# Performance work log

Hardware: AMD Instinct MI355X
Metric: run time of the kernel (lower is better)

## Reference

```python
import jax, jax.numpy as jnp
import numpy as np
import math

INPUT_DIM = 1024
DIM_K = 1024
DIM_V = 1024
B, N = 4, 2048

def setup_inputs() -> dict:
    key = jax.random.key(0)
    ks = jax.random.split(key, 7)
    s = 1.0 / math.sqrt(INPUT_DIM)
    return {
        'x':  jax.random.normal(ks[0], (B, N, INPUT_DIM), dtype=jnp.float32),
        'Wq': jax.random.uniform(ks[1], (DIM_K, INPUT_DIM), jnp.float32, -s, s),
        'bq': jax.random.uniform(ks[2], (DIM_K,), jnp.float32, -s, s),
        'Wk': jax.random.uniform(ks[3], (DIM_K, INPUT_DIM), jnp.float32, -s, s),
        'bk': jax.random.uniform(ks[4], (DIM_K,), jnp.float32, -s, s),
        'Wv': jax.random.uniform(ks[5], (DIM_V, INPUT_DIM), jnp.float32, -s, s),
        'bv': jax.random.uniform(ks[6], (DIM_V,), jnp.float32, -s, s),
    }

def reference(x, Wq, bq, Wk, bk, Wv, bv):
    norm_fact = 1.0 / math.sqrt(DIM_K)
    # torch Linear: y = x @ W.T + b
    Q = jnp.einsum('bnd,kd->bnk', x, Wq) + bq  # [B,N,dim_k]
    K = jnp.einsum('bnd,kd->bnk', x, Wk) + bk  # [B,N,dim_k]
    V = jnp.einsum('bnd,vd->bnv', x, Wv) + bv  # [B,N,dim_v]
    scores = jnp.einsum('bqk,bnk->bqn', Q, K)  # [B,N,N]
    # NOTE: original code applies softmax FIRST, then scales by norm_fact
    atten = jax.nn.softmax(scores, axis=-1) * norm_fact
    return jnp.einsum('bqn,bnv->bqv', atten, V)  # [B,N,dim_v]
```

## Files before the change

### kernel.cpp

```cpp
#include <hip/hip_runtime.h>


typedef _Float16 hfx8 __attribute__((ext_vector_type(8)));
typedef _Float16 hfx4 __attribute__((ext_vector_type(4)));
typedef float fx4 __attribute__((ext_vector_type(4)));

__device__ __forceinline__ void load_lds16(const void* g, void* l) {
    __builtin_amdgcn_global_load_lds(
        (const __attribute__((address_space(1))) void*)g,
        (__attribute__((address_space(3))) void*)l, 16, 0, 0);
}

template <int N> __device__ __forceinline__ void vmwait() {
    if constexpr (N == 8) asm volatile("s_waitcnt vmcnt(8)" ::: "memory");
    else asm volatile("s_waitcnt vmcnt(0)" ::: "memory");
}

__device__ __forceinline__ void xcd_remap(int& x, int& y, int& z) {
    const int gx = gridDim.x, gy = gridDim.y;
    const int lin = blockIdx.x + gx * (blockIdx.y + gy * blockIdx.z);
    const int cpx = (gx * gy * gridDim.z) >> 3;
    const int w = (lin & 7) * cpx + (lin >> 3);
    x = w % gx;
    y = (w / gx) % gy;
    z = w / (gx * gy);
}

__global__ __launch_bounds__(256) void conv_all_kernel(
    const float4* __restrict__ x, _Float16* __restrict__ xs,
    const float4* __restrict__ w0, const float4* __restrict__ w1, const float4* __restrict__ w2,
    _Float16* __restrict__ o0, _Float16* __restrict__ o1, _Float16* __restrict__ o2)
{
    const int b = blockIdx.x;
    const float4* in;
    _Float16* out;
    long i;
    if (b < 8192) {
        in = x; out = xs;
        i = (long)b * 256 + threadIdx.x;
    } else {
        const int wi = b - 8192;
        const int wsel = wi >> 10;
        in = wsel == 0 ? w0 : (wsel == 1 ? w1 : w2);
        out = wsel == 0 ? o0 : (wsel == 1 ? o1 : o2);
        i = (long)(wi & 1023) * 256 + threadIdx.x;
    }
    float4 v = in[i];
    hfx4 h;
    h[0] = (_Float16)v.x; h[1] = (_Float16)v.y;
    h[2] = (_Float16)v.z; h[3] = (_Float16)v.w;
    *(hfx4*)&out[i * 4] = h;
}

template <int OMODE>
__global__ __launch_bounds__(256, 2) void gemm2(
    const _Float16* __restrict__ A,
    const _Float16* __restrict__ Bq, const _Float16* __restrict__ Bk, const _Float16* __restrict__ Bv,
    const float* __restrict__ bq, const float* __restrict__ bk, const float* __restrict__ bv,
    float* __restrict__ outF, _Float16* __restrict__ oQ, _Float16* __restrict__ oK, _Float16* __restrict__ oV,
    int K, int lda, int ldb, int ldc, float alpha,
    long sAz, long sBz, long sCz)
{
    constexpr int BM = 128, BN = 128, BK = 64;
    constexpr int LPT = 8;

    __shared__ __attribute__((aligned(16))) _Float16 lds[2][(BM + BN) * BK];

    int bx, by, z;
    xcd_remap(bx, by, z);

    A += (long)z * sAz;
    const _Float16* B = (OMODE == 1) ? (z == 0 ? Bq : (z == 1 ? Bk : Bv))
                                     : Bq + (long)z * sBz;

    const int tid = threadIdx.x;
    const int lane = tid & 63;
    const int wv = tid >> 6;
    const int wr = wv >> 1, wc = wv & 1;
    const int lr = lane & 15, lk = lane >> 4;

    const long m0 = (long)by * BM;
    const long n0 = (long)bx * BN;

    fx4 acc[4][4] = {};

    auto STAGE = [&](int kt, int b) {
#pragma unroll
        for (int i = 0; i < LPT; ++i) {
            const int c = i * 256 + tid;
            if (i < 4) {
                const int row = c >> 3, slot = c & 7;
                load_lds16(A + (m0 + row) * (long)lda + kt + ((slot ^ (row & 7)) << 3),
                           &lds[b][c * 8]);
            } else {
                const int c2 = c - 1024;
                const int row = c2 >> 3, slot = c2 & 7;
                load_lds16(B + (n0 + row) * (long)ldb + kt + ((slot ^ (row & 7)) << 3),
                           &lds[b][BM * BK + c2 * 8]);
            }
        }
    };

    const int NT = K / BK;
    STAGE(0, 0);
    STAGE(BK, 1);
    vmwait<8>();
    __builtin_amdgcn_s_barrier();
    __builtin_amdgcn_sched_barrier(0);

    const int rA0 = wr * 64 + lr;
    const int rB0 = wc * 64 + lr;
    const int eA = (rA0 & 7) << 3;
    const int eB = (rB0 & 7) << 3;

    for (int t = 0; t < NT; ++t) {
        const _Float16* LA = &lds[t & 1][0];
        const _Float16* LB = LA + BM * BK;

        hfx8 bfr[4][2];
#pragma unroll
        for (int nf = 0; nf < 4; ++nf)
#pragma unroll
            for (int ks = 0; ks < 2; ++ks)
                bfr[nf][ks] = *(const hfx8*)&LB[(rB0 + nf * 16) * BK + ((ks * 32 + lk * 8) ^ eB)];

#pragma unroll
        for (int q = 0; q < 4; ++q) {
            hfx8 afr[2];
#pragma unroll
            for (int ks = 0; ks < 2; ++ks)
                afr[ks] = *(const hfx8*)&LA[(rA0 + q * 16) * BK + ((ks * 32 + lk * 8) ^ eA)];
            __builtin_amdgcn_s_setprio(1);
#pragma unroll
            for (int nf = 0; nf < 4; ++nf)
#pragma unroll
                for (int ks = 0; ks < 2; ++ks)
                    acc[q][nf] = __builtin_amdgcn_mfma_f32_16x16x32_f16(
                        afr[ks], bfr[nf][ks], acc[q][nf], 0, 0, 0);
            __builtin_amdgcn_s_setprio(0);
        }

        __builtin_amdgcn_s_barrier();
        if (t + 2 < NT) {
            STAGE((t + 2) * BK, t & 1);
            vmwait<8>();
        } else {
            vmwait<0>();
        }
        __builtin_amdgcn_s_barrier();
        __builtin_amdgcn_sched_barrier(0);
    }

#pragma unroll
    for (int mf = 0; mf < 4; ++mf) {
#pragma unroll
        for (int nf = 0; nf < 4; ++nf) {
            const long row0 = m0 + wr * 64 + mf * 16 + lk * 4;
            const long col = n0 + wc * 64 + nf * 16 + lr;
            if constexpr (OMODE == 0) {
                float* oz = outF + (long)z * sCz;
#pragma unroll
                for (int j = 0; j < 4; ++j)
                    oz[(row0 + j) * (long)ldc + col] = alpha * acc[mf][nf][j];
            } else if constexpr (OMODE == 2) {
                _Float16* oz = oQ + (long)z * sCz;
#pragma unroll
                for (int j = 0; j < 4; ++j)
                    oz[(row0 + j) * (long)ldc + col] = (_Float16)(alpha * acc[mf][nf][j]);
            } else {
                if (z == 0) {
                    const float bb = bq[col];
#pragma unroll
                    for (int j = 0; j < 4; ++j)
                        oQ[(row0 + j) * 1024 + col] = (_Float16)(acc[mf][nf][j] + bb);
                } else if (z == 1) {
                    const float bb = bk[col];
#pragma unroll
                    for (int j = 0; j < 4; ++j)
                        oK[(row0 + j) * 1024 + col] = (_Float16)(acc[mf][nf][j] + bb);
                } else {
                    const float bb = bv[col];
                    hfx4 pk;
#pragma unroll
                    for (int j = 0; j < 4; ++j) pk[j] = (_Float16)(acc[mf][nf][j] + bb);
                    *(hfx4*)&oV[((row0 >> 11) * 1024 + col) * 2048 + (row0 & 2047)] = pk;
                }
            }
        }
    }
}

__global__ __launch_bounds__(256) void softmax_kernel(_Float16* __restrict__ S)
{
    const long row = blockIdx.x;
    _Float16* r = S + row * 2048;
    const int t = threadIdx.x;

    const hfx8 hv = *(const hfx8*)&r[t * 8];
    float v[8];
#pragma unroll
    for (int j = 0; j < 8; ++j) v[j] = (float)hv[j];

    float mx = v[0];
#pragma unroll
    for (int j = 1; j < 8; ++j) mx = fmaxf(mx, v[j]);
#pragma unroll
    for (int o = 32; o; o >>= 1) mx = fmaxf(mx, __shfl_xor(mx, o, 64));

    __shared__ float redm[4];
    __shared__ float reds[4];
    const int w = t >> 6;
    if ((t & 63) == 0) redm[w] = mx;
    __syncthreads();
    mx = fmaxf(fmaxf(redm[0], redm[1]), fmaxf(redm[2], redm[3]));

    float e[8];
    float s = 0.f;
#pragma unroll
    for (int j = 0; j < 8; ++j) {
        e[j] = __expf(v[j] - mx);
        s += e[j];
    }
#pragma unroll
    for (int o = 32; o; o >>= 1) s += __shfl_xor(s, o, 64);
    if ((t & 63) == 0) reds[w] = s;
    __syncthreads();
    s = reds[0] + reds[1] + reds[2] + reds[3];

    const float inv = 1.0f / s;
    hfx8 p;
#pragma unroll
    for (int j = 0; j < 8; ++j) p[j] = (_Float16)(e[j] * inv);
    *(hfx8*)&r[t * 8] = p;
}

extern "C" void kernel_launch(void* const* d_in, const int* in_sizes, int n_in,
                              void* d_out, int out_size, void* d_ws, size_t ws_size,
                              hipStream_t stream)
{
    const float* x  = (const float*)d_in[0];
    const float* Wq = (const float*)d_in[1];
    const float* bq = (const float*)d_in[2];
    const float* Wk = (const float*)d_in[3];
    const float* bk = (const float*)d_in[4];
    const float* Wv = (const float*)d_in[5];
    const float* bv = (const float*)d_in[6];
    float* out = (float*)d_out;

    _Float16* xs  = (_Float16*)d_ws;
    _Float16* Wqh = xs + 8192ull * 1024;
    _Float16* Wkh = Wqh + 1024ull * 1024;
    _Float16* Wvh = Wkh + 1024ull * 1024;
    _Float16* Qp  = Wvh + 1024ull * 1024;
    _Float16* Ks  = Qp + 8192ull * 1024;
    _Float16* Vt  = Ks + 8192ull * 1024;
    _Float16* Sh  = Vt + 4ull * 1024 * 2048;

    dim3 blk(256);

    conv_all_kernel<<<11264, blk, 0, stream>>>(
        (const float4*)x, xs,
        (const float4*)Wq, (const float4*)Wk, (const float4*)Wv, Wqh, Wkh, Wvh);

    gemm2<1><<<dim3(8, 64, 3), blk, 0, stream>>>(
        xs, Wqh, Wkh, Wvh, bq, bk, bv,
        nullptr, Qp, Ks, Vt,
        1024, 1024, 1024, 0, 1.0f, 0L, 0L, 0L);

    gemm2<2><<<dim3(16, 16, 4), blk, 0, stream>>>(
        Qp, Ks, nullptr, nullptr, nullptr, nullptr, nullptr,
        nullptr, Sh, nullptr, nullptr,
        1024, 1024, 1024, 2048, 1.0f,
        2097152L, 2097152L, 4194304L);

    softmax_kernel<<<2048 * 4, blk, 0, stream>>>(Sh);

    gemm2<0><<<dim3(8, 16, 4), blk, 0, stream>>>(
        Sh, Vt, nullptr, nullptr, nullptr, nullptr, nullptr,
        out, nullptr, nullptr, nullptr,
        2048, 2048, 2048, 1024, 0.03125f,
        4194304L, 2097152L, 2097152L);
}
```

Baseline: 171.8 us.

## Fuse Q/K/V projections into one GEMM kernel sharing the x tile

Replaces the z-indexed QKV projection launch (three separate 128x128 tiles per block over z) with a dedicated kernel in which each block loads one x tile and the matching tiles of Wq, Wk and Wv. It computes all three outputs with 48 accumulator fragments per wave and BK reduced to 32. The goal is to cut x tile reloads from global memory by a factor of three and to raise MFMA work per A-fragment load. The cost is much higher register pressure (192 accumulator floats per thread), which under launch_bounds(256,2) could cause spills or lower occupancy. The grid also shrinks to 512 blocks.

```diff
diff --git a/kernel.cpp b/kernel.cpp
--- a/kernel.cpp
+++ b/kernel.cpp
@@ -52,12 +52,128 @@
     *(hfx4*)&out[i * 4] = h;
 }
 
-template <int OMODE>
-__global__ __launch_bounds__(256, 2) void gemm2(
+__global__ __launch_bounds__(256, 2) void gemmQKV(
     const _Float16* __restrict__ A,
     const _Float16* __restrict__ Bq, const _Float16* __restrict__ Bk, const _Float16* __restrict__ Bv,
     const float* __restrict__ bq, const float* __restrict__ bk, const float* __restrict__ bv,
-    float* __restrict__ outF, _Float16* __restrict__ oQ, _Float16* __restrict__ oK, _Float16* __restrict__ oV,
+    _Float16* __restrict__ oQ, _Float16* __restrict__ oK, _Float16* __restrict__ oV)
+{
+    constexpr int BK = 32;
+    __shared__ __attribute__((aligned(16))) _Float16 lds[2][4 * 128 * BK];
+
+    int bx, by, zz;
+    xcd_remap(bx, by, zz);
+
+    const int tid = threadIdx.x;
+    const int lane = tid & 63;
+    const int wv = tid >> 6;
+    const int wr = wv >> 1, wc = wv & 1;
+    const int lr = lane & 15, lk = lane >> 4;
+
+    const long m0 = (long)by * 128;
+    const long n0 = (long)bx * 128;
+
+    fx4 acc[3][4][4] = {};
+
+    auto STAGE = [&](int kt, int b) {
+#pragma unroll
+        for (int i = 0; i < 8; ++i) {
+            const int slot = tid & 3;
+            if (i < 2) {
+                const int row = i * 64 + (tid >> 2);
+                load_lds16(A + (m0 + row) * 1024L + kt + ((slot ^ ((row >> 1) & 3)) << 3),
+                           &lds[b][row * BK + slot * 8]);
+            } else {
+                const int which = (i - 2) >> 1;
+                const int row = ((i - 2) & 1) * 64 + (tid >> 2);
+                const _Float16* Bsel = which == 0 ? Bq : (which == 1 ? Bk : Bv);
+                load_lds16(Bsel + (n0 + row) * 1024L + kt + ((slot ^ ((row >> 1) & 3)) << 3),
+                           &lds[b][(1 + which) * 4096 + row * BK + slot * 8]);
+            }
+        }
+    };
+
+    const int NT = 1024 / BK;
+    STAGE(0, 0);
+    STAGE(BK, 1);
+    vmwait<8>();
+    __builtin_amdgcn_s_barrier();
+    __builtin_amdgcn_sched_barrier(0);
+
+    const int rA0 = wr * 64 + lr;
+    const int rB0 = wc * 64 + lr;
+    const int eA = (((rA0 >> 1) & 3) << 3);
+    const int eB = (((rB0 >> 1) & 3) << 3);
+
+    for (int t = 0; t < NT; ++t) {
+        const _Float16* L = &lds[t & 1][0];
+
+        hfx8 afr[4];
+#pragma unroll
+        for (int q = 0; q < 4; ++q)
+            afr[q] = *(const hfx8*)&L[(rA0 + q * 16) * BK + ((lk * 8) ^ eA)];
+
+#pragma unroll
+        for (int w3 = 0; w3 < 3; ++w3) {
+            hfx8 bfr[4];
+#pragma unroll
+            for (int nf = 0; nf < 4; ++nf)
+                bfr[nf] = *(const hfx8*)&L[(1 + w3) * 4096 + (rB0 + nf * 16) * BK + ((lk * 8) ^ eB)];
+            __builtin_amdgcn_s_setprio(1);
+#pragma unroll
+            for (int q = 0; q < 4; ++q)
+#pragma unroll
+                for (int nf = 0; nf < 4; ++nf)
+                    acc[w3][q][nf] = __builtin_amdgcn_mfma_f32_16x16x32_f16(
+                        afr[q], bfr[nf], acc[w3][q][nf], 0, 0, 0);
+            __builtin_amdgcn_s_setprio(0);
+        }
+
+        __builtin_amdgcn_s_barrier();
+        if (t + 2 < NT) {
+            STAGE((t + 2) * BK, t & 1);
+            vmwait<8>();
+        } else {
+            vmwait<0>();
+        }
+        __builtin_amdgcn_s_barrier();
+        __builtin_amdgcn_sched_barrier(0);
+    }
+
+#pragma unroll
+    for (int w3 = 0; w3 < 3; ++w3) {
+#pragma unroll
+        for (int mf = 0; mf < 4; ++mf) {
+#pragma unroll
+            for (int nf = 0; nf < 4; ++nf) {
+                const long row0 = m0 + wr * 64 + mf * 16 + lk * 4;
+                const long col = n0 + wc * 64 + nf * 16 + lr;
+                if (w3 == 0) {
+                    const float bb = bq[col];
+#pragma unroll
+                    for (int j = 0; j < 4; ++j)
+                        oQ[(row0 + j) * 1024 + col] = (_Float16)(acc[0][mf][nf][j] + bb);
+                } else if (w3 == 1) {
+                    const float bb = bk[col];
+#pragma unroll
+                    for (int j = 0; j < 4; ++j)
+                        oK[(row0 + j) * 1024 + col] = (_Float16)(acc[1][mf][nf][j] + bb);
+                } else {
+                    const float bb = bv[col];
+                    hfx4 pk;
+#pragma unroll
+                    for (int j = 0; j < 4; ++j) pk[j] = (_Float16)(acc[2][mf][nf][j] + bb);
+                    *(hfx4*)&oV[((row0 >> 11) * 1024 + col) * 2048 + (row0 & 2047)] = pk;
+                }
+            }
+        }
+    }
+}
+
+template <int OMODE>
+__global__ __launch_bounds__(256, 2) void gemm2(
+    const _Float16* __restrict__ A, const _Float16* __restrict__ Bq,
+    float* __restrict__ outF, _Float16* __restrict__ oH,
     int K, int lda, int ldb, int ldc, float alpha,
     long sAz, long sBz, long sCz)
 {
@@ -70,8 +186,7 @@
     xcd_remap(bx, by, z);
 
     A += (long)z * sAz;
-    const _Float16* B = (OMODE == 1) ? (z == 0 ? Bq : (z == 1 ? Bk : Bv))
-                                     : Bq + (long)z * sBz;
+    const _Float16* B = Bq + (long)z * sBz;
 
     const int tid = threadIdx.x;
     const int lane = tid & 63;
@@ -162,29 +277,11 @@
 #pragma unroll
                 for (int j = 0; j < 4; ++j)
                     oz[(row0 + j) * (long)ldc + col] = alpha * acc[mf][nf][j];
-            } else if constexpr (OMODE == 2) {
-                _Float16* oz = oQ + (long)z * sCz;
+            } else {
+                _Float16* oz = oH + (long)z * sCz;
 #pragma unroll
                 for (int j = 0; j < 4; ++j)
                     oz[(row0 + j) * (long)ldc + col] = (_Float16)(alpha * acc[mf][nf][j]);
-            } else {
-                if (z == 0) {
-                    const float bb = bq[col];
-#pragma unroll
-                    for (int j = 0; j < 4; ++j)
-                        oQ[(row0 + j) * 1024 + col] = (_Float16)(acc[mf][nf][j] + bb);
-                } else if (z == 1) {
-                    const float bb = bk[col];
-#pragma unroll
-                    for (int j = 0; j < 4; ++j)
-                        oK[(row0 + j) * 1024 + col] = (_Float16)(acc[mf][nf][j] + bb);
-                } else {
-                    const float bb = bv[col];
-                    hfx4 pk;
-#pragma unroll
-                    for (int j = 0; j < 4; ++j) pk[j] = (_Float16)(acc[mf][nf][j] + bb);
-                    *(hfx4*)&oV[((row0 >> 11) * 1024 + col) * 2048 + (row0 & 2047)] = pk;
-                }
             }
         }
     }
@@ -262,22 +359,18 @@
         (const float4*)x, xs,
         (const float4*)Wq, (const float4*)Wk, (const float4*)Wv, Wqh, Wkh, Wvh);
 
-    gemm2<1><<<dim3(8, 64, 3), blk, 0, stream>>>(
-        xs, Wqh, Wkh, Wvh, bq, bk, bv,
-        nullptr, Qp, Ks, Vt,
-        1024, 1024, 1024, 0, 1.0f, 0L, 0L, 0L);
+    gemmQKV<<<dim3(8, 64, 1), blk, 0, stream>>>(
+        xs, Wqh, Wkh, Wvh, bq, bk, bv, Qp, Ks, Vt);
 
     gemm2<2><<<dim3(16, 16, 4), blk, 0, stream>>>(
-        Qp, Ks, nullptr, nullptr, nullptr, nullptr, nullptr,
-        nullptr, Sh, nullptr, nullptr,
+        Qp, Ks, nullptr, Sh,
         1024, 1024, 1024, 2048, 1.0f,
         2097152L, 2097152L, 4194304L);
 
     softmax_kernel<<<2048 * 4, blk, 0, stream>>>(Sh);
 
     gemm2<0><<<dim3(8, 16, 4), blk, 0, stream>>>(
-        Sh, Vt, nullptr, nullptr, nullptr, nullptr, nullptr,
-        out, nullptr, nullptr, nullptr,
+        Sh, Vt, out, nullptr,
         2048, 2048, 2048, 1024, 0.03125f,
         4194304L, 2097152L, 2097152L);
 }
```

Result: faster. 156.7 us (-8.8%).
